# Performance work log

Measured on AMD Instinct MI355X. Metric: run time of the kernel, lower is better.

## Reference

```python
import jax, jax.numpy as jnp
import numpy as np

N_LAYERS = 2
D_MODEL = 1024
D_INNER = 2048  # expand=2
D_STATE = 16
D_CONV = 4
DT_RANK = 64    # ceil(d_model/16)
N_CLASSES = 10
B, L = 4, 1024


def setup_inputs() -> dict:
    key = jax.random.key(0)
    ks = jax.random.split(key, 20)
    s = 0.02
    inp = {
        'x': jax.random.normal(ks[0], (B, L, D_MODEL), jnp.float32),
        'ln1_w': jnp.ones((N_LAYERS, D_MODEL), jnp.float32),
        'ln1_b': jnp.zeros((N_LAYERS, D_MODEL), jnp.float32),
        'in_proj_w': jax.random.normal(ks[1], (N_LAYERS, 2 * D_INNER, D_MODEL), jnp.float32) * s,
        'conv_w': jax.random.normal(ks[2], (N_LAYERS, D_INNER, D_CONV), jnp.float32) * 0.2,
        'conv_b': jnp.zeros((N_LAYERS, D_INNER), jnp.float32),
        'x_proj_w': jax.random.normal(ks[3], (N_LAYERS, DT_RANK + 2 * D_STATE, D_INNER), jnp.float32) * s,
        'dt_proj_w': jax.random.normal(ks[4], (N_LAYERS, D_INNER, DT_RANK), jnp.float32) * 0.1,
        'dt_proj_b': jax.random.normal(ks[5], (N_LAYERS, D_INNER), jnp.float32) * 0.1 - 4.6,  # softplus -> dt ~ 0.01
        'A_log': jnp.broadcast_to(jnp.log(jnp.arange(1, D_STATE + 1, dtype=jnp.float32)), (N_LAYERS, D_INNER, D_STATE)) + 0.0,
        'D_param': jnp.ones((N_LAYERS, D_INNER), jnp.float32),
        'out_proj_w': jax.random.normal(ks[6], (N_LAYERS, D_MODEL, D_INNER), jnp.float32) * s,
        'norm_w': jnp.ones((D_MODEL,), jnp.float32),
        'norm_b': jnp.zeros((D_MODEL,), jnp.float32),
        'head_w': jax.random.normal(ks[7], (N_CLASSES, D_MODEL), jnp.float32) * s,
        'head_b': jnp.zeros((N_CLASSES,), jnp.float32),
    }
    return inp


def _layernorm(x, w, b, eps=1e-5):
    mu = jnp.mean(x, axis=-1, keepdims=True)
    var = jnp.var(x, axis=-1, keepdims=True)
    return (x - mu) * jax.lax.rsqrt(var + eps) * w + b


def _selective_scan(xc, dt, A, Bm, Cm, D):
    # xc, dt: (B, L, D_INNER); Bm, Cm: (B, L, D_STATE); A: (D_INNER, D_STATE); D: (D_INNER,)
    def step(h, inp):
        dt_t, B_t, C_t, xc_t = inp  # (B,C),(B,N),(B,N),(B,C)
        dA = jnp.exp(dt_t[..., None] * A)            # (B, C, N)
        h = dA * h + (dt_t * xc_t)[..., None] * B_t[:, None, :]
        y = jnp.einsum('bcn,bn->bc', h, C_t)
        return h, y

    h0 = jnp.zeros((xc.shape[0], A.shape[0], A.shape[1]), xc.dtype)
    xs = (dt.transpose(1, 0, 2), Bm.transpose(1, 0, 2), Cm.transpose(1, 0, 2), xc.transpose(1, 0, 2))
    _, ys = jax.lax.scan(step, h0, xs)
    y = ys.transpose(1, 0, 2)  # (B, L, C)
    return y + xc * D


def _mamba_layer(x, ln_w, ln_b, in_w, cw, cb, xp_w, dtp_w, dtp_b, A_log, D, out_w):
    h = _layernorm(x, ln_w, ln_b)
    xz = jnp.einsum('bld,ed->ble', h, in_w)          # (B, L, 2*D_INNER)
    x_in, z = jnp.split(xz, 2, axis=-1)
    # causal depthwise conv1d, kernel D_CONV
    xp = jnp.pad(x_in, ((0, 0), (D_CONV - 1, 0), (0, 0)))
    conv = cb
    for k in range(D_CONV):
        conv = conv + cw[:, k] * xp[:, k:k + x_in.shape[1], :]
    xc = jax.nn.silu(conv)
    x_dbl = jnp.einsum('blc,ec->ble', xc, xp_w)
    dt_r = x_dbl[..., :DT_RANK]
    Bm = x_dbl[..., DT_RANK:DT_RANK + D_STATE]
    Cm = x_dbl[..., DT_RANK + D_STATE:]
    dt = jax.nn.softplus(jnp.einsum('blr,cr->blc', dt_r, dtp_w) + dtp_b)
    A = -jnp.exp(A_log)
    y = _selective_scan(xc, dt, A, Bm, Cm, D)
    y = y * jax.nn.silu(z)
    return x + jnp.einsum('blc,dc->bld', y, out_w)


def reference(x, ln1_w, ln1_b, in_proj_w, conv_w, conv_b, x_proj_w, dt_proj_w, dt_proj_b,
              A_log, D_param, out_proj_w, norm_w, norm_b, head_w, head_b):
    for i in range(N_LAYERS):
        x = _mamba_layer(x, ln1_w[i], ln1_b[i], in_proj_w[i], conv_w[i], conv_b[i],
                         x_proj_w[i], dt_proj_w[i], dt_proj_b[i], A_log[i], D_param[i], out_proj_w[i])
    x = _layernorm(x, norm_w, norm_b)
    pooled = jnp.mean(x, axis=1)  # (B, D_MODEL)
    return pooled @ head_w.T + head_b
```

## Files before the change

### kernel.cpp

```cpp
#include <hip/hip_runtime.h>
#include <hip/hip_bf16.h>

#define N_LAYERS 2
#define D_MODEL 1024
#define D_INNER 2048
#define D_STATE 16
#define D_CONV 4
#define DT_RANK 64
#define N_CLASSES 10
#define BB 4
#define LL 1024
#define BL (BB*LL)
#define CH 32
#define CLEN (LL/CH)
#define KS 8
#define KSO 2

typedef __attribute__((ext_vector_type(8))) short bf16x8;
typedef __attribute__((ext_vector_type(8))) unsigned short us8;
typedef __attribute__((ext_vector_type(4))) float f32x4;

typedef const void __attribute__((address_space(1)))* gas_ptr;
typedef void __attribute__((address_space(3)))* las_ptr;
#define GLDS16(g, p) __builtin_amdgcn_global_load_lds((gas_ptr)(g), (las_ptr)(p), 16, 0, 0)

__device__ inline unsigned short rnd_bf16(float x) {
  unsigned u = __float_as_uint(x);
  return (unsigned short)((u + 0x7FFFu + ((u >> 16) & 1u)) >> 16);
}
__device__ inline float b2f(unsigned short u) {
  return __uint_as_float(((unsigned)u) << 16);
}

__global__ __launch_bounds__(256) void round_k(const float* __restrict__ in,
    unsigned short* __restrict__ hi) {
  const int i = blockIdx.x * 256 + threadIdx.x;
  const float4 v = ((const float4*)in)[i];
  ushort4 h4;
  h4.x = rnd_bf16(v.x); h4.y = rnd_bf16(v.y);
  h4.z = rnd_bf16(v.z); h4.w = rnd_bf16(v.w);
  ((ushort4*)hi)[i] = h4;
}

__global__ __launch_bounds__(256) void layernorm_bf16_k(const float* __restrict__ x,
    const float* __restrict__ w, const float* __restrict__ b,
    unsigned short* __restrict__ oh) {
  const int row = blockIdx.x;
  const int t = threadIdx.x;
  const float4 v = *(const float4*)(x + (size_t)row * D_MODEL + t * 4);
  float s = v.x + v.y + v.z + v.w;
  float q = v.x*v.x + v.y*v.y + v.z*v.z + v.w*v.w;
  #pragma unroll
  for (int o = 32; o; o >>= 1) { s += __shfl_down(s, o); q += __shfl_down(q, o); }
  __shared__ float red[8];
  if ((t & 63) == 0) { red[t >> 6] = s; red[4 + (t >> 6)] = q; }
  __syncthreads();
  s = red[0] + red[1] + red[2] + red[3];
  q = red[4] + red[5] + red[6] + red[7];
  const float mean = s * (1.f / D_MODEL);
  const float var  = q * (1.f / D_MODEL) - mean * mean;
  const float rstd = rsqrtf(var + 1e-5f);
  const float4 wv = *(const float4*)(w + t * 4);
  const float4 bv = *(const float4*)(b + t * 4);
  ushort4 h4;
  h4.x = rnd_bf16((v.x - mean) * rstd * wv.x + bv.x);
  h4.y = rnd_bf16((v.y - mean) * rstd * wv.y + bv.y);
  h4.z = rnd_bf16((v.z - mean) * rstd * wv.z + bv.z);
  h4.w = rnd_bf16((v.w - mean) * rstd * wv.w + bv.w);
  ((ushort4*)(oh + (size_t)row * D_MODEL))[t] = h4;
}

template<int OUT>
__global__ __launch_bounds__(256) void oreduce_ln_k(
    const float* __restrict__ part, const float* __restrict__ Xin,
    float* __restrict__ Xout,
    const float* __restrict__ w, const float* __restrict__ b,
    void* __restrict__ out) {
  const int row = blockIdx.x;
  const int t = threadIdx.x;
  float4 v = *(const float4*)(Xin + (size_t)row * D_MODEL + t * 4);
  #pragma unroll
  for (int k = 0; k < KSO; k++) {
    const float4 p = *(const float4*)(part + (size_t)k * BL * D_MODEL
                                      + (size_t)row * D_MODEL + t * 4);
    v.x += p.x; v.y += p.y; v.z += p.z; v.w += p.w;
  }
  *(float4*)(Xout + (size_t)row * D_MODEL + t * 4) = v;
  float s = v.x + v.y + v.z + v.w;
  float q = v.x*v.x + v.y*v.y + v.z*v.z + v.w*v.w;
  #pragma unroll
  for (int o = 32; o; o >>= 1) { s += __shfl_down(s, o); q += __shfl_down(q, o); }
  __shared__ float red[8];
  if ((t & 63) == 0) { red[t >> 6] = s; red[4 + (t >> 6)] = q; }
  __syncthreads();
  s = red[0] + red[1] + red[2] + red[3];
  q = red[4] + red[5] + red[6] + red[7];
  const float mean = s * (1.f / D_MODEL);
  const float var  = q * (1.f / D_MODEL) - mean * mean;
  const float rstd = rsqrtf(var + 1e-5f);
  const float4 wv = *(const float4*)(w + t * 4);
  const float4 bv = *(const float4*)(b + t * 4);
  float4 o4;
  o4.x = (v.x - mean) * rstd * wv.x + bv.x;
  o4.y = (v.y - mean) * rstd * wv.y + bv.y;
  o4.z = (v.z - mean) * rstd * wv.z + bv.z;
  o4.w = (v.w - mean) * rstd * wv.w + bv.w;
  if constexpr (OUT == 0) {
    ushort4 h4;
    h4.x = rnd_bf16(o4.x); h4.y = rnd_bf16(o4.y);
    h4.z = rnd_bf16(o4.z); h4.w = rnd_bf16(o4.w);
    ((ushort4*)((unsigned short*)out + (size_t)row * D_MODEL))[t] = h4;
  } else {
    *(float4*)((float*)out + (size_t)row * D_MODEL + t * 4) = o4;
  }
}

__global__ __launch_bounds__(512) void mfma_gemm256_nt(
    const unsigned short* __restrict__ A, const unsigned short* __restrict__ B,
    unsigned short* __restrict__ C, int K, int ldc) {
  __shared__ unsigned short S[65536];
  const int tid = threadIdx.x;
  const int l = tid & 63;
  const int w = tid >> 6;
  const int wm = w >> 2, wn = w & 3;
  const int bid = blockIdx.y * 16 + blockIdx.x;
  const int x = bid & 7, v = bid >> 3;
  const int bx = (x & 1) * 8 + (v & 7);
  const int by = (x >> 1) * 4 + (v >> 3);
  const int m0 = by * 256, n0 = bx * 256;
  const int nkt = K >> 6;
  const int r8 = (tid >> 3) & 7;
  const int c16s = (tid & 7) ^ r8;

  auto stage1 = [&](int kt, int mat, int half) {
    const unsigned short* base = (mat == 0) ? (A + (size_t)m0 * K)
                                            : (B + (size_t)n0 * K);
    unsigned short* dst = S + ((kt & 1) * 32768 + mat * 16384 + half * 8192);
    #pragma unroll
    for (int e = 0; e < 2; ++e) {
      const int row = half * 128 + e * 64 + (tid >> 3);
      GLDS16(base + (size_t)row * K + kt * 64 + c16s * 8,
             dst + e * 4096 + tid * 8);
    }
  };
  auto stage_full = [&](int kt) {
    stage1(kt, 0, 0); stage1(kt, 0, 1); stage1(kt, 1, 0); stage1(kt, 1, 1);
  };

  stage_full(0);
  if (nkt > 1) stage_full(1);

  f32x4 acc[8][4] = {};
  const int fr = l & 15;
  const int fk8 = l >> 4;

  #pragma unroll 1
  for (int kt = 0; kt < nkt; ++kt) {
    if (kt + 1 < nkt) asm volatile("s_waitcnt vmcnt(8)" ::: "memory");
    else              asm volatile("s_waitcnt vmcnt(0)" ::: "memory");
    __builtin_amdgcn_s_barrier();
    __builtin_amdgcn_sched_barrier(0);
    const unsigned short* SA = S + (kt & 1) * 32768;
    const unsigned short* SB = SA + 16384;
    #pragma unroll
    for (int kk8 = 0; kk8 < 8; kk8 += 4) {
      bf16x8 av[8], bv[4];
      const int c8 = kk8 + fk8;
      #pragma unroll
      for (int i = 0; i < 8; ++i) {
        const int R = wm * 128 + i * 16 + fr;
        av[i] = *(const bf16x8*)&SA[R * 64 + ((c8 ^ (R & 7)) << 3)];
      }
      #pragma unroll
      for (int j = 0; j < 4; ++j) {
        const int R = wn * 64 + j * 16 + fr;
        bv[j] = *(const bf16x8*)&SB[R * 64 + ((c8 ^ (R & 7)) << 3)];
      }
      __builtin_amdgcn_s_setprio(1);
      #pragma unroll
      for (int i = 0; i < 8; ++i)
        #pragma unroll
        for (int j = 0; j < 4; ++j)
          acc[i][j] = __builtin_amdgcn_mfma_f32_16x16x32_bf16(
              av[i], bv[j], acc[i][j], 0, 0, 0);
      __builtin_amdgcn_s_setprio(0);
    }
    __builtin_amdgcn_s_barrier();
    __builtin_amdgcn_sched_barrier(0);
    if (kt + 2 < nkt) stage_full(kt + 2);
  }

  const int orow = (l >> 4) * 4, ocol = l & 15;
  #pragma unroll
  for (int i = 0; i < 8; ++i)
    #pragma unroll
    for (int j = 0; j < 4; ++j)
      #pragma unroll
      for (int r = 0; r < 4; ++r) {
        const int m = m0 + wm * 128 + i * 16 + orow + r;
        const int n = n0 + wn * 64 + j * 16 + ocol;
        C[(size_t)m * ldc + n] = rnd_bf16(acc[i][j][r]);
      }
}

template<int EPI, int KSEG>
__global__ __launch_bounds__(256) void mfma_gemm_nt(
    const unsigned short* __restrict__ Ah, const unsigned short* __restrict__ Bh,
    void* __restrict__ Cv, int M, int N, int K, int ldc,
    const float* __restrict__ bias) {
  __shared__ unsigned short As[128 * 64];
  __shared__ unsigned short Bs[128 * 64];
  const int tid = threadIdx.x;
  const int w = tid >> 6, l = tid & 63;
  const int wr = w >> 1, wc = w & 1;
  const int nbx = gridDim.x;
  const int nwg = nbx * gridDim.y;
  int bid = blockIdx.y * nbx + blockIdx.x;
  bid = (bid & 7) * (nwg >> 3) + (bid >> 3);
  const int st = bid >> 6, wi = bid & 63;
  const int stpr = (nbx >= 8) ? (nbx >> 3) : 1;
  int n0, m0;
  if (nbx >= 8) {
    n0 = ((st % stpr) * 8 + (wi & 7)) * 128;
    m0 = ((st / stpr) * 8 + (wi >> 3)) * 128;
  } else {
    n0 = (bid % nbx) * 128;
    m0 = (bid / nbx) * 128;
  }
  const int kz = (KSEG > 1) ? blockIdx.z : 0;
  const int kbeg = kz * (K / KSEG);
  const int kend = kbeg + K / KSEG;
  const int srow = l >> 3;
  const int scol = (l & 7) * 8;
  const int fr = l & 15;
  const int fk = (l >> 4) * 8;
  f32x4 acc[4][4] = {};

  #pragma unroll 1
  for (int k0 = kbeg; k0 < kend; k0 += 64) {
    __syncthreads();
    #pragma unroll
    for (int it = 0; it < 4; ++it) {
      const int bi = it * 4 + w;
      const int row = bi * 8 + srow;
      GLDS16(Ah + (size_t)(m0 + row) * K + k0 + scol, &As[bi * 512 + l * 8]);
      GLDS16(Bh + (size_t)(n0 + row) * K + k0 + scol, &Bs[bi * 512 + l * 8]);
    }
    __syncthreads();
    #pragma unroll
    for (int kk = 0; kk < 64; kk += 32) {
      bf16x8 a[4], b[4];
      #pragma unroll
      for (int f = 0; f < 4; ++f)
        b[f] = *(const bf16x8*)&Bs[(wc * 64 + f * 16 + fr) * 64 + kk + fk];
      #pragma unroll
      for (int f = 0; f < 4; ++f)
        a[f] = *(const bf16x8*)&As[(wr * 64 + f * 16 + fr) * 64 + kk + fk];
      #pragma unroll
      for (int i = 0; i < 4; ++i)
        #pragma unroll
        for (int j = 0; j < 4; ++j)
          acc[i][j] = __builtin_amdgcn_mfma_f32_16x16x32_bf16(
              a[i], b[j], acc[i][j], 0, 0, 0);
    }
  }
  const int orow = (l >> 4) * 4;
  const int ocol = l & 15;
  if constexpr (EPI == 0 || EPI == 2) {
    unsigned short* Cw = (unsigned short*)Cv;
    #pragma unroll
    for (int i = 0; i < 4; ++i)
      #pragma unroll
      for (int j = 0; j < 4; ++j)
        #pragma unroll
        for (int r = 0; r < 4; ++r) {
          const int m = m0 + wr * 64 + i * 16 + orow + r;
          const int n = n0 + wc * 64 + j * 16 + ocol;
          float vv = acc[i][j][r];
          if constexpr (EPI == 2) {
            vv += bias[n];
            vv = (vv > 20.f) ? vv : log1pf(__expf(vv));
          }
          Cw[(size_t)m * ldc + n] = rnd_bf16(vv);
        }
  } else {
    float* Cw = (float*)Cv + (size_t)kz * M * ldc;
    #pragma unroll
    for (int i = 0; i < 4; ++i)
      #pragma unroll
      for (int j = 0; j < 4; ++j)
        #pragma unroll
        for (int r = 0; r < 4; ++r) {
          const int m = m0 + wr * 64 + i * 16 + orow + r;
          const int n = n0 + wc * 64 + j * 16 + ocol;
          Cw[(size_t)m * ldc + n] = acc[i][j][r];
        }
  }
}

__global__ __launch_bounds__(256) void sgemm_splitk_k(
    const unsigned short* __restrict__ A, const float* __restrict__ B,
    float* __restrict__ part) {
  __shared__ float As[32][64 + 4];
  __shared__ float Bs[32][32 + 4];
  const int tid = threadIdx.x;
  const int n0 = blockIdx.x * 32;
  const int m0 = blockIdx.y * 64;
  const int kz = blockIdx.z;
  const int tn = (tid & 15) * 2;
  const int tm = (tid >> 4) * 4;
  float acc[4][2] = {};
  for (int kb = 0; kb < 256; kb += 32) {
    const int k0 = kz * 256 + kb;
    {
      int r = tid >> 2, c8 = (tid & 3) * 8;
      us8 u = *(const us8*)(A + (size_t)(m0 + r) * D_INNER + k0 + c8);
      #pragma unroll
      for (int j = 0; j < 8; j++) As[c8 + j][r] = b2f((unsigned short)u[j]);
    }
    {
      int r = tid >> 3, c4 = tid & 7;
      float4 v = *(const float4*)(B + (size_t)(n0 + r) * D_INNER + k0 + c4 * 4);
      Bs[c4*4+0][r] = v.x; Bs[c4*4+1][r] = v.y;
      Bs[c4*4+2][r] = v.z; Bs[c4*4+3][r] = v.w;
    }
    __syncthreads();
    #pragma unroll
    for (int k = 0; k < 32; k++) {
      float a[4], bf[2];
      #pragma unroll
      for (int i = 0; i < 4; i++) a[i] = As[k][tm + i];
      bf[0] = Bs[k][tn]; bf[1] = Bs[k][tn + 1];
      #pragma unroll
      for (int i = 0; i < 4; i++) {
        acc[i][0] = fmaf(a[i], bf[0], acc[i][0]);
        acc[i][1] = fmaf(a[i], bf[1], acc[i][1]);
      }
    }
    __syncthreads();
  }
  float* p = part + (size_t)kz * BL * 96;
  #pragma unroll
  for (int i = 0; i < 4; i++) {
    const int m = m0 + tm + i;
    p[(size_t)m * 96 + n0 + tn]     = acc[i][0];
    p[(size_t)m * 96 + n0 + tn + 1] = acc[i][1];
  }
}

__global__ __launch_bounds__(256) void xproj_reduce_k(
    const float* __restrict__ part, unsigned short* __restrict__ dtr,
    float* __restrict__ bc) {
  const int i = blockIdx.x * 256 + threadIdx.x;
  const int m = i / 96, col = i % 96;
  float s = 0.f;
  #pragma unroll
  for (int k = 0; k < KS; k++) s += part[(size_t)k * BL * 96 + i];
  if (col < DT_RANK) dtr[(size_t)m * DT_RANK + col] = rnd_bf16(s);
  else               bc[(size_t)m * 32 + (col - DT_RANK)] = s;
}

__global__ __launch_bounds__(256) void conv_silu_k(
    const unsigned short* __restrict__ xz,
    const float* __restrict__ cw, const float* __restrict__ cb,
    unsigned short* __restrict__ xc) {
  const int gid = blockIdx.x * 256 + threadIdx.x;
  const int c4 = (gid & (D_INNER / 4 - 1)) << 2;
  const int row = gid >> 9;
  const int l = row & (LL - 1);
  const unsigned short* base = xz + (size_t)row * (2 * D_INNER) + c4;
  const float4 w0 = *(const float4*)(cw + (c4 + 0) * 4);
  const float4 w1 = *(const float4*)(cw + (c4 + 1) * 4);
  const float4 w2 = *(const float4*)(cw + (c4 + 2) * 4);
  const float4 w3 = *(const float4*)(cw + (c4 + 3) * 4);
  float4 acc = *(const float4*)(cb + c4);
  ushort4 uv = *(const ushort4*)base;
  acc.x = fmaf(w0.w, b2f(uv.x), acc.x); acc.y = fmaf(w1.w, b2f(uv.y), acc.y);
  acc.z = fmaf(w2.w, b2f(uv.z), acc.z); acc.w = fmaf(w3.w, b2f(uv.w), acc.w);
  if (l >= 1) {
    uv = *(const ushort4*)(base - 2 * D_INNER);
    acc.x = fmaf(w0.z, b2f(uv.x), acc.x); acc.y = fmaf(w1.z, b2f(uv.y), acc.y);
    acc.z = fmaf(w2.z, b2f(uv.z), acc.z); acc.w = fmaf(w3.z, b2f(uv.w), acc.w);
  }
  if (l >= 2) {
    uv = *(const ushort4*)(base - 4 * D_INNER);
    acc.x = fmaf(w0.y, b2f(uv.x), acc.x); acc.y = fmaf(w1.y, b2f(uv.y), acc.y);
    acc.z = fmaf(w2.y, b2f(uv.z), acc.z); acc.w = fmaf(w3.y, b2f(uv.w), acc.w);
  }
  if (l >= 3) {
    uv = *(const ushort4*)(base - 6 * D_INNER);
    acc.x = fmaf(w0.x, b2f(uv.x), acc.x); acc.y = fmaf(w1.x, b2f(uv.y), acc.y);
    acc.z = fmaf(w2.x, b2f(uv.z), acc.z); acc.w = fmaf(w3.x, b2f(uv.w), acc.w);
  }
  ushort4 o4;
  o4.x = rnd_bf16(acc.x / (1.f + __expf(-acc.x)));
  o4.y = rnd_bf16(acc.y / (1.f + __expf(-acc.y)));
  o4.z = rnd_bf16(acc.z / (1.f + __expf(-acc.z)));
  o4.w = rnd_bf16(acc.w / (1.f + __expf(-acc.w)));
  *(ushort4*)(xc + (size_t)row * D_INNER + c4) = o4;
}

__device__ inline void wpowers(float w1, float* P) {
  const float w2 = w1 * w1, w3 = w2 * w1, w4 = w2 * w2;
  const float w5 = w4 * w1, w6 = w4 * w2, w7 = w4 * w3, w8 = w4 * w4;
  P[0] = w1;  P[1] = w2;  P[2] = w3;  P[3] = w4;
  P[4] = w5;  P[5] = w6;  P[6] = w7;  P[7] = w8;
  P[8]  = w8 * w1;  P[9]  = w8 * w2;  P[10] = w8 * w3;  P[11] = w8 * w4;
  P[12] = w8 * w5;  P[13] = w8 * w6;  P[14] = w8 * w7;  P[15] = w8 * w8;
}

__global__ __launch_bounds__(256) void scan_pass1_k(
    const unsigned short* __restrict__ dt, const unsigned short* __restrict__ xc,
    const float* __restrict__ bc, const float* __restrict__ A_log,
    float* __restrict__ hend, float* __restrict__ sumdt) {
  const int c = blockIdx.x * 256 + threadIdx.x;
  const int k = blockIdx.y;
  const int b = blockIdx.z;
  float Ac[D_STATE];
  bool fast = true;
  #pragma unroll
  for (int n = 0; n < D_STATE; n++) {
    Ac[n] = -__expf(A_log[c * D_STATE + n]);
    fast = fast && (fabsf(Ac[n] + (float)(n + 1)) <= 4e-6f * (float)(n + 1));
  }
  float h[D_STATE] = {};
  float sd = 0.f;
  const size_t r0 = (size_t)b * LL + (size_t)k * CLEN;
  const unsigned short* dtp = dt + r0 * D_INNER + c;
  const unsigned short* xcp = xc + r0 * D_INNER + c;
  const float* Bp  = bc + r0 * 32;

  float dtv = b2f(dtp[0]);
  float xv  = b2f(xcp[0]);
  float4 B0 = *(const float4*)(Bp + 0);
  float4 B1 = *(const float4*)(Bp + 4);
  float4 B2 = *(const float4*)(Bp + 8);
  float4 B3 = *(const float4*)(Bp + 12);
  if (fast) {
    for (int l = 0; l < CLEN; l++) {
      const int lp = (l + 1 < CLEN) ? l + 1 : l;
      const float dtv2 = b2f(dtp[(size_t)lp * D_INNER]);
      const float xv2  = b2f(xcp[(size_t)lp * D_INNER]);
      const float4 B0n = *(const float4*)(Bp + (size_t)lp * 32 + 0);
      const float4 B1n = *(const float4*)(Bp + (size_t)lp * 32 + 4);
      const float4 B2n = *(const float4*)(Bp + (size_t)lp * 32 + 8);
      const float4 B3n = *(const float4*)(Bp + (size_t)lp * 32 + 12);
      sd += dtv;
      const float dx = dtv * xv;
      float P[D_STATE];
      wpowers(__expf(-dtv), P);
      const float Bv[D_STATE] = {B0.x,B0.y,B0.z,B0.w, B1.x,B1.y,B1.z,B1.w,
                                 B2.x,B2.y,B2.z,B2.w, B3.x,B3.y,B3.z,B3.w};
      #pragma unroll
      for (int n = 0; n < D_STATE; n++)
        h[n] = fmaf(P[n], h[n], dx * Bv[n]);
      dtv = dtv2; xv = xv2; B0 = B0n; B1 = B1n; B2 = B2n; B3 = B3n;
    }
  } else {
    for (int l = 0; l < CLEN; l++) {
      const int lp = (l + 1 < CLEN) ? l + 1 : l;
      const float dtv2 = b2f(dtp[(size_t)lp * D_INNER]);
      const float xv2  = b2f(xcp[(size_t)lp * D_INNER]);
      const float4 B0n = *(const float4*)(Bp + (size_t)lp * 32 + 0);
      const float4 B1n = *(const float4*)(Bp + (size_t)lp * 32 + 4);
      const float4 B2n = *(const float4*)(Bp + (size_t)lp * 32 + 8);
      const float4 B3n = *(const float4*)(Bp + (size_t)lp * 32 + 12);
      sd += dtv;
      const float dx = dtv * xv;
      const float Bv[D_STATE] = {B0.x,B0.y,B0.z,B0.w, B1.x,B1.y,B1.z,B1.w,
                                 B2.x,B2.y,B2.z,B2.w, B3.x,B3.y,B3.z,B3.w};
      #pragma unroll
      for (int n = 0; n < D_STATE; n++)
        h[n] = fmaf(__expf(dtv * Ac[n]), h[n], dx * Bv[n]);
      dtv = dtv2; xv = xv2; B0 = B0n; B1 = B1n; B2 = B2n; B3 = B3n;
    }
  }
  float* he = hend + (((size_t)(b * CH + k) * D_INNER + c) << 4);
  #pragma unroll
  for (int n = 0; n < D_STATE; n += 4)
    *(float4*)(he + n) = make_float4(h[n], h[n+1], h[n+2], h[n+3]);
  sumdt[(size_t)(b * CH + k) * D_INNER + c] = sd;
}

__global__ __launch_bounds__(256) void scan_fix_k(
    float* __restrict__ hend, const float* __restrict__ sumdt,
    const float* __restrict__ A_log) {
  const int gid = blockIdx.x * 256 + threadIdx.x;
  const int n = gid & 15;
  const int c = (gid >> 4) & (D_INNER - 1);
  const int b = gid >> 15;
  const float Ac = -__expf(A_log[c * D_STATE + n]);
  float hrun = 0.f;
  for (int k = 0; k < CH; k++) {
    const size_t base = (size_t)(b * CH + k) * D_INNER + c;
    const float sd = sumdt[base];
    float* hp = hend + (base << 4) + n;
    const float tmp = *hp;
    *hp = hrun;
    hrun = fmaf(__expf(Ac * sd), hrun, tmp);
  }
}

__global__ __launch_bounds__(256) void scan_pass3_k(
    const unsigned short* __restrict__ dt, const unsigned short* __restrict__ xc,
    const float* __restrict__ bc, const unsigned short* __restrict__ xz,
    const float* __restrict__ h0, const float* __restrict__ A_log,
    const float* __restrict__ Dp, unsigned short* __restrict__ yh) {
  const int c = blockIdx.x * 256 + threadIdx.x;
  const int k = blockIdx.y;
  const int b = blockIdx.z;
  float Ac[D_STATE];
  bool fast = true;
  #pragma unroll
  for (int n = 0; n < D_STATE; n++) {
    Ac[n] = -__expf(A_log[c * D_STATE + n]);
    fast = fast && (fabsf(Ac[n] + (float)(n + 1)) <= 4e-6f * (float)(n + 1));
  }
  const float Dv = Dp[c];
  float h[D_STATE];
  const float* hp = h0 + (((size_t)(b * CH + k) * D_INNER + c) << 4);
  #pragma unroll
  for (int n = 0; n < D_STATE; n += 4) {
    const float4 v = *(const float4*)(hp + n);
    h[n] = v.x; h[n+1] = v.y; h[n+2] = v.z; h[n+3] = v.w;
  }
  const size_t r0 = (size_t)b * LL + (size_t)k * CLEN;
  const unsigned short* dtp = dt + r0 * D_INNER + c;
  const unsigned short* xcp = xc + r0 * D_INNER + c;
  const float* Bp  = bc + r0 * 32;
  const unsigned short* zp = xz + r0 * (size_t)(2 * D_INNER) + D_INNER + c;
  unsigned short* yhp = yh + r0 * D_INNER + c;

  float dtv = b2f(dtp[0]);
  float xv  = b2f(xcp[0]);
  float zv  = b2f(zp[0]);
  float4 B0 = *(const float4*)(Bp + 0);
  float4 B1 = *(const float4*)(Bp + 4);
  float4 B2 = *(const float4*)(Bp + 8);
  float4 B3 = *(const float4*)(Bp + 12);
  float4 C0 = *(const float4*)(Bp + 16);
  float4 C1 = *(const float4*)(Bp + 20);
  float4 C2 = *(const float4*)(Bp + 24);
  float4 C3 = *(const float4*)(Bp + 28);
  if (fast) {
    for (int l = 0; l < CLEN; l++) {
      const int lp = (l + 1 < CLEN) ? l + 1 : l;
      const float dtv2 = b2f(dtp[(size_t)lp * D_INNER]);
      const float xv2  = b2f(xcp[(size_t)lp * D_INNER]);
      const float zv2  = b2f(zp[(size_t)lp * 2 * D_INNER]);
      const float4 B0n = *(const float4*)(Bp + (size_t)lp * 32 + 0);
      const float4 B1n = *(const float4*)(Bp + (size_t)lp * 32 + 4);
      const float4 B2n = *(const float4*)(Bp + (size_t)lp * 32 + 8);
      const float4 B3n = *(const float4*)(Bp + (size_t)lp * 32 + 12);
      const float4 C0n = *(const float4*)(Bp + (size_t)lp * 32 + 16);
      const float4 C1n = *(const float4*)(Bp + (size_t)lp * 32 + 20);
      const float4 C2n = *(const float4*)(Bp + (size_t)lp * 32 + 24);
      const float4 C3n = *(const float4*)(Bp + (size_t)lp * 32 + 28);
      const float dx = dtv * xv;
      float P[D_STATE];
      wpowers(__expf(-dtv), P);
      const float Bv[D_STATE] = {B0.x,B0.y,B0.z,B0.w, B1.x,B1.y,B1.z,B1.w,
                                 B2.x,B2.y,B2.z,B2.w, B3.x,B3.y,B3.z,B3.w};
      const float Cv[D_STATE] = {C0.x,C0.y,C0.z,C0.w, C1.x,C1.y,C1.z,C1.w,
                                 C2.x,C2.y,C2.z,C2.w, C3.x,C3.y,C3.z,C3.w};
      float y = 0.f;
      #pragma unroll
      for (int n = 0; n < D_STATE; n++) {
        h[n] = fmaf(P[n], h[n], dx * Bv[n]);
        y = fmaf(h[n], Cv[n], y);
      }
      y = fmaf(xv, Dv, y);
      y *= zv / (1.f + __expf(-zv));
      yhp[(size_t)l * D_INNER] = rnd_bf16(y);
      dtv = dtv2; xv = xv2; zv = zv2;
      B0 = B0n; B1 = B1n; B2 = B2n; B3 = B3n;
      C0 = C0n; C1 = C1n; C2 = C2n; C3 = C3n;
    }
  } else {
    for (int l = 0; l < CLEN; l++) {
      const int lp = (l + 1 < CLEN) ? l + 1 : l;
      const float dtv2 = b2f(dtp[(size_t)lp * D_INNER]);
      const float xv2  = b2f(xcp[(size_t)lp * D_INNER]);
      const float zv2  = b2f(zp[(size_t)lp * 2 * D_INNER]);
      const float4 B0n = *(const float4*)(Bp + (size_t)lp * 32 + 0);
      const float4 B1n = *(const float4*)(Bp + (size_t)lp * 32 + 4);
      const float4 B2n = *(const float4*)(Bp + (size_t)lp * 32 + 8);
      const float4 B3n = *(const float4*)(Bp + (size_t)lp * 32 + 12);
      const float4 C0n = *(const float4*)(Bp + (size_t)lp * 32 + 16);
      const float4 C1n = *(const float4*)(Bp + (size_t)lp * 32 + 20);
      const float4 C2n = *(const float4*)(Bp + (size_t)lp * 32 + 24);
      const float4 C3n = *(const float4*)(Bp + (size_t)lp * 32 + 28);
      const float dx = dtv * xv;
      const float Bv[D_STATE] = {B0.x,B0.y,B0.z,B0.w, B1.x,B1.y,B1.z,B1.w,
                                 B2.x,B2.y,B2.z,B2.w, B3.x,B3.y,B3.z,B3.w};
      const float Cv[D_STATE] = {C0.x,C0.y,C0.z,C0.w, C1.x,C1.y,C1.z,C1.w,
                                 C2.x,C2.y,C2.z,C2.w, C3.x,C3.y,C3.z,C3.w};
      float y = 0.f;
      #pragma unroll
      for (int n = 0; n < D_STATE; n++) {
        h[n] = fmaf(__expf(dtv * Ac[n]), h[n], dx * Bv[n]);
        y = fmaf(h[n], Cv[n], y);
      }
      y = fmaf(xv, Dv, y);
      y *= zv / (1.f + __expf(-zv));
      yhp[(size_t)l * D_INNER] = rnd_bf16(y);
      dtv = dtv2; xv = xv2; zv = zv2;
      B0 = B0n; B1 = B1n; B2 = B2n; B3 = B3n;
      C0 = C0n; C1 = C1n; C2 = C2n; C3 = C3n;
    }
  }
}

__global__ __launch_bounds__(256) void pool1_k(const float* __restrict__ h,
    float* __restrict__ pp) {
  const int d = blockIdx.x * 256 + threadIdx.x;
  const int b = blockIdx.y;
  const int seg = blockIdx.z;
  float s = 0.f;
  const size_t base = (size_t)b * LL + (size_t)seg * 64;
  for (int l = 0; l < 64; l++) s += h[(base + l) * D_MODEL + d];
  pp[((size_t)(b * 16 + seg)) * D_MODEL + d] = s;
}
__global__ __launch_bounds__(256) void pool2_k(const float* __restrict__ pp,
    float* __restrict__ pooled) {
  const int d = blockIdx.x * 256 + threadIdx.x;
  const int b = blockIdx.y;
  float s = 0.f;
  #pragma unroll
  for (int k = 0; k < 16; k++) s += pp[((size_t)(b * 16 + k)) * D_MODEL + d];
  pooled[b * D_MODEL + d] = s * (1.f / LL);
}

__global__ __launch_bounds__(64) void head_k(const float* __restrict__ pooled,
    const float* __restrict__ hw, const float* __restrict__ hb,
    float* __restrict__ out) {
  const int b = blockIdx.x / N_CLASSES;
  const int j = blockIdx.x % N_CLASSES;
  float s = 0.f;
  for (int k = threadIdx.x; k < D_MODEL; k += 64)
    s = fmaf(pooled[b * D_MODEL + k], hw[j * D_MODEL + k], s);
  #pragma unroll
  for (int o = 32; o; o >>= 1) s += __shfl_down(s, o);
  if (threadIdx.x == 0) out[b * N_CLASSES + j] = s + hb[j];
}

extern "C" void kernel_launch(void* const* d_in, const int* in_sizes, int n_in,
                              void* d_out, int out_size, void* d_ws, size_t ws_size,
                              hipStream_t stream) {
  const float* x0    = (const float*)d_in[0];
  const float* ln1w  = (const float*)d_in[1];
  const float* ln1b  = (const float*)d_in[2];
  const float* inw   = (const float*)d_in[3];
  const float* convw = (const float*)d_in[4];
  const float* convb = (const float*)d_in[5];
  const float* xpw   = (const float*)d_in[6];
  const float* dtpw  = (const float*)d_in[7];
  const float* dtpb  = (const float*)d_in[8];
  const float* Alog  = (const float*)d_in[9];
  const float* Dp    = (const float*)d_in[10];
  const float* outw  = (const float*)d_in[11];
  const float* normw = (const float*)d_in[12];
  const float* normb = (const float*)d_in[13];
  const float* headw = (const float*)d_in[14];
  const float* headb = (const float*)d_in[15];

  float* ws = (float*)d_ws;
  size_t f = 0;
  float* X      = ws + f; f += (size_t)BL * D_MODEL;
  float* xzf    = ws + f; f += (size_t)BL * D_INNER;
  float* bc     = ws + f; f += (size_t)BL * 32;
  float* dty    = ws + f; f += (size_t)BL * D_INNER;
  float* pooled = ws + f; f += 4096;
  float* pooldp = ws + f; f += (size_t)16 * BB * D_MODEL;
  float* xpart  = ws + f; f += (size_t)KS * BL * 96;
  float* hend   = ws + f; f += (size_t)BB * CH * D_INNER * D_STATE;
  float* opart  = ws + f; f += (size_t)KSO * BL * D_MODEL;
  unsigned short* hh  = (unsigned short*)(ws + f); f += (size_t)BL * D_MODEL / 2;
  unsigned short* yh  = (unsigned short*)(ws + f); f += (size_t)BL * D_INNER / 2;
  unsigned short* xcb = (unsigned short*)(ws + f); f += (size_t)BL * D_INNER / 2;
  unsigned short* dtr = (unsigned short*)(ws + f); f += (size_t)BL * DT_RANK / 2;
  unsigned short* wih = (unsigned short*)(ws + f);
  f += (size_t)N_LAYERS * 2 * D_INNER * D_MODEL / 2;
  unsigned short* woh = (unsigned short*)(ws + f);
  f += (size_t)N_LAYERS * D_MODEL * D_INNER / 2;
  unsigned short* wdt = (unsigned short*)(ws + f);
  f += (size_t)N_LAYERS * D_INNER * DT_RANK / 2;
  unsigned short* xz  = (unsigned short*)xzf;
  unsigned short* dtb = (unsigned short*)dty;
  float* sumdt = xpart;

  round_k<<<(N_LAYERS * 2 * D_INNER * D_MODEL) / 1024, 256, 0, stream>>>(inw, wih);
  round_k<<<(N_LAYERS * D_MODEL * D_INNER) / 1024, 256, 0, stream>>>(outw, woh);
  round_k<<<(N_LAYERS * D_INNER * DT_RANK) / 1024, 256, 0, stream>>>(dtpw, wdt);
  layernorm_bf16_k<<<BL, 256, 0, stream>>>(x0, ln1w, ln1b, hh);

  for (int layer = 0; layer < N_LAYERS; ++layer) {
    const unsigned short* wi = wih + (size_t)layer * 2 * D_INNER * D_MODEL;
    const unsigned short* wo = woh + (size_t)layer * D_MODEL * D_INNER;
    const unsigned short* wd = wdt + (size_t)layer * D_INNER * DT_RANK;
    mfma_gemm256_nt<<<dim3(16, 16), 512, 0, stream>>>(
        hh, wi, xz, D_MODEL, 2 * D_INNER);
    conv_silu_k<<<(BL * D_INNER / 4) / 256, 256, 0, stream>>>(
        xz, convw + layer * D_INNER * D_CONV, convb + layer * D_INNER, xcb);
    sgemm_splitk_k<<<dim3(96 / 32, 4096 / 64, KS), 256, 0, stream>>>(
        xcb, xpw + (size_t)layer * 96 * D_INNER, xpart);
    xproj_reduce_k<<<(BL * 96) / 256, 256, 0, stream>>>(xpart, dtr, bc);
    mfma_gemm_nt<2, 1><<<dim3(2048 / 128, 4096 / 128), 256, 0, stream>>>(
        dtr, wd, dtb, BL, D_INNER, DT_RANK, D_INNER, dtpb + layer * D_INNER);
    scan_pass1_k<<<dim3(D_INNER / 256, CH, BB), 256, 0, stream>>>(
        dtb, xcb, bc, Alog + (size_t)layer * D_INNER * D_STATE, hend, sumdt);
    scan_fix_k<<<(BB * D_INNER * D_STATE) / 256, 256, 0, stream>>>(
        hend, sumdt, Alog + (size_t)layer * D_INNER * D_STATE);
    scan_pass3_k<<<dim3(D_INNER / 256, CH, BB), 256, 0, stream>>>(
        dtb, xcb, bc, xz, hend, Alog + (size_t)layer * D_INNER * D_STATE,
        Dp + layer * D_INNER, yh);
    mfma_gemm_nt<1, KSO><<<dim3(1024 / 128, 4096 / 128, KSO), 256, 0, stream>>>(
        yh, wo, opart, BL, D_MODEL, D_INNER, D_MODEL, nullptr);
    const float* Xin = (layer == 0) ? x0 : X;
    if (layer + 1 < N_LAYERS) {
      oreduce_ln_k<0><<<BL, 256, 0, stream>>>(
          opart, Xin, X, ln1w + (layer + 1) * D_MODEL,
          ln1b + (layer + 1) * D_MODEL, hh);
    } else {
      oreduce_ln_k<1><<<BL, 256, 0, stream>>>(opart, Xin, X, normw, normb, dty);
    }
  }

  pool1_k<<<dim3(D_MODEL / 256, BB, 16), 256, 0, stream>>>(dty, pooldp);
  pool2_k<<<dim3(D_MODEL / 256, BB), 256, 0, stream>>>(pooldp, pooled);
  head_k<<<BB * N_CLASSES, 64, 0, stream>>>(pooled, headw, headb, (float*)d_out);
}
```

Baseline: 504.9 us.

## Move out_proj onto 256-tile split-K GEMM and overlap next-stage loads with MFMAs

The 256x256 MFMA GEMM is templated to support a float split-K epilogue and an unremapped grid, and out_proj now uses it with four K-segments instead of the 128-tile kernel with two. Inside the main loop, the second k-half's LDS fragments are loaded first, then the barrier and next-stage global-to-LDS loads are issued before the second MFMA batch, so loads overlap compute. The workspace is reordered so the larger split-K partial buffer aliases the xz/xcb/hend region, which is dead by then. The cost is double the fp32 partial write and reduce traffic.

```diff
diff --git a/kernel.cpp b/kernel.cpp
--- a/kernel.cpp
+++ b/kernel.cpp
@@ -14,7 +14,7 @@
 #define CH 32
 #define CLEN (LL/CH)
 #define KS 8
-#define KSO 2
+#define KSO 4
 
 typedef __attribute__((ext_vector_type(8))) short bf16x8;
 typedef __attribute__((ext_vector_type(8))) unsigned short us8;
@@ -115,20 +115,28 @@
   }
 }
 
+template<int EPI, int KSEG, int REMAP>
 __global__ __launch_bounds__(512) void mfma_gemm256_nt(
     const unsigned short* __restrict__ A, const unsigned short* __restrict__ B,
-    unsigned short* __restrict__ C, int K, int ldc) {
+    void* __restrict__ Cv, int M, int N, int K, int ldc) {
   __shared__ unsigned short S[65536];
   const int tid = threadIdx.x;
   const int l = tid & 63;
   const int w = tid >> 6;
   const int wm = w >> 2, wn = w & 3;
-  const int bid = blockIdx.y * 16 + blockIdx.x;
-  const int x = bid & 7, v = bid >> 3;
-  const int bx = (x & 1) * 8 + (v & 7);
-  const int by = (x >> 1) * 4 + (v >> 3);
+  int bx, by;
+  if constexpr (REMAP == 1) {
+    const int bid = blockIdx.y * 16 + blockIdx.x;
+    const int x = bid & 7, v = bid >> 3;
+    bx = (x & 1) * 8 + (v & 7);
+    by = (x >> 1) * 4 + (v >> 3);
+  } else {
+    bx = blockIdx.x; by = blockIdx.y;
+  }
   const int m0 = by * 256, n0 = bx * 256;
-  const int nkt = K >> 6;
+  const int kseg = K / KSEG;
+  const int kbeg = (KSEG > 1) ? blockIdx.z * kseg : 0;
+  const int nkt = kseg >> 6;
   const int r8 = (tid >> 3) & 7;
   const int c16s = (tid & 7) ^ r8;
 
@@ -139,7 +147,7 @@
     #pragma unroll
     for (int e = 0; e < 2; ++e) {
       const int row = half * 128 + e * 64 + (tid >> 3);
-      GLDS16(base + (size_t)row * K + kt * 64 + c16s * 8,
+      GLDS16(base + (size_t)row * K + kbeg + kt * 64 + c16s * 8,
              dst + e * 4096 + tid * 8);
     }
   };
@@ -162,10 +170,9 @@
     __builtin_amdgcn_sched_barrier(0);
     const unsigned short* SA = S + (kt & 1) * 32768;
     const unsigned short* SB = SA + 16384;
-    #pragma unroll
-    for (int kk8 = 0; kk8 < 8; kk8 += 4) {
-      bf16x8 av[8], bv[4];
-      const int c8 = kk8 + fk8;
+    bf16x8 av[8], bv[4];
+    {
+      const int c8 = fk8;
       #pragma unroll
       for (int i = 0; i < 8; ++i) {
         const int R = wm * 128 + i * 16 + fr;
@@ -185,22 +192,59 @@
               av[i], bv[j], acc[i][j], 0, 0, 0);
       __builtin_amdgcn_s_setprio(0);
     }
-    __builtin_amdgcn_s_barrier();
-    __builtin_amdgcn_sched_barrier(0);
-    if (kt + 2 < nkt) stage_full(kt + 2);
+    {
+      const int c8 = 4 + fk8;
+      #pragma unroll
+      for (int i = 0; i < 8; ++i) {
+        const int R = wm * 128 + i * 16 + fr;
+        av[i] = *(const bf16x8*)&SA[R * 64 + ((c8 ^ (R & 7)) << 3)];
+      }
+      #pragma unroll
+      for (int j = 0; j < 4; ++j) {
+        const int R = wn * 64 + j * 16 + fr;
+        bv[j] = *(const bf16x8*)&SB[R * 64 + ((c8 ^ (R & 7)) << 3)];
+      }
+      asm volatile("s_waitcnt lgkmcnt(0)" ::: "memory");
+      __builtin_amdgcn_s_barrier();
+      __builtin_amdgcn_sched_barrier(0);
+      if (kt + 2 < nkt) stage_full(kt + 2);
+      __builtin_amdgcn_s_setprio(1);
+      #pragma unroll
+      for (int i = 0; i < 8; ++i)
+        #pragma unroll
+        for (int j = 0; j < 4; ++j)
+          acc[i][j] = __builtin_amdgcn_mfma_f32_16x16x32_bf16(
+              av[i], bv[j], acc[i][j], 0, 0, 0);
+      __builtin_amdgcn_s_setprio(0);
+    }
   }
 
   const int orow = (l >> 4) * 4, ocol = l & 15;
-  #pragma unroll
-  for (int i = 0; i < 8; ++i)
+  if constexpr (EPI == 0) {
+    unsigned short* C = (unsigned short*)Cv;
     #pragma unroll
-    for (int j = 0; j < 4; ++j)
-      #pragma unroll
-      for (int r = 0; r < 4; ++r) {
-        const int m = m0 + wm * 128 + i * 16 + orow + r;
-        const int n = n0 + wn * 64 + j * 16 + ocol;
-        C[(size_t)m * ldc + n] = rnd_bf16(acc[i][j][r]);
-      }
+    for (int i = 0; i < 8; ++i)
+      #pragma unroll
+      for (int j = 0; j < 4; ++j)
+        #pragma unroll
+        for (int r = 0; r < 4; ++r) {
+          const int m = m0 + wm * 128 + i * 16 + orow + r;
+          const int n = n0 + wn * 64 + j * 16 + ocol;
+          C[(size_t)m * ldc + n] = rnd_bf16(acc[i][j][r]);
+        }
+  } else {
+    float* C = (float*)Cv + (size_t)blockIdx.z * M * ldc;
+    #pragma unroll
+    for (int i = 0; i < 8; ++i)
+      #pragma unroll
+      for (int j = 0; j < 4; ++j)
+        #pragma unroll
+        for (int r = 0; r < 4; ++r) {
+          const int m = m0 + wm * 128 + i * 16 + orow + r;
+          const int n = n0 + wn * 64 + j * 16 + ocol;
+          C[(size_t)m * ldc + n] = acc[i][j][r];
+        }
+  }
 }
 
 template<int EPI, int KSEG>
@@ -668,16 +712,17 @@
   size_t f = 0;
   float* X      = ws + f; f += (size_t)BL * D_MODEL;
   float* xzf    = ws + f; f += (size_t)BL * D_INNER;
+  unsigned short* xcb = (unsigned short*)(ws + f);
+  f += (size_t)BL * D_INNER / 2;
+  float* hend   = ws + f; f += (size_t)BB * CH * D_INNER * D_STATE;
+  float* opart  = xzf;
   float* bc     = ws + f; f += (size_t)BL * 32;
   float* dty    = ws + f; f += (size_t)BL * D_INNER;
   float* pooled = ws + f; f += 4096;
   float* pooldp = ws + f; f += (size_t)16 * BB * D_MODEL;
   float* xpart  = ws + f; f += (size_t)KS * BL * 96;
-  float* hend   = ws + f; f += (size_t)BB * CH * D_INNER * D_STATE;
-  float* opart  = ws + f; f += (size_t)KSO * BL * D_MODEL;
   unsigned short* hh  = (unsigned short*)(ws + f); f += (size_t)BL * D_MODEL / 2;
   unsigned short* yh  = (unsigned short*)(ws + f); f += (size_t)BL * D_INNER / 2;
-  unsigned short* xcb = (unsigned short*)(ws + f); f += (size_t)BL * D_INNER / 2;
   unsigned short* dtr = (unsigned short*)(ws + f); f += (size_t)BL * DT_RANK / 2;
   unsigned short* wih = (unsigned short*)(ws + f);
   f += (size_t)N_LAYERS * 2 * D_INNER * D_MODEL / 2;
@@ -698,8 +743,8 @@
     const unsigned short* wi = wih + (size_t)layer * 2 * D_INNER * D_MODEL;
     const unsigned short* wo = woh + (size_t)layer * D_MODEL * D_INNER;
     const unsigned short* wd = wdt + (size_t)layer * D_INNER * DT_RANK;
-    mfma_gemm256_nt<<<dim3(16, 16), 512, 0, stream>>>(
-        hh, wi, xz, D_MODEL, 2 * D_INNER);
+    mfma_gemm256_nt<0, 1, 1><<<dim3(16, 16), 512, 0, stream>>>(
+        hh, wi, xz, BL, 2 * D_INNER, D_MODEL, 2 * D_INNER);
     conv_silu_k<<<(BL * D_INNER / 4) / 256, 256, 0, stream>>>(
         xz, convw + layer * D_INNER * D_CONV, convb + layer * D_INNER, xcb);
     sgemm_splitk_k<<<dim3(96 / 32, 4096 / 64, KS), 256, 0, stream>>>(
@@ -714,8 +759,9 @@
     scan_pass3_k<<<dim3(D_INNER / 256, CH, BB), 256, 0, stream>>>(
         dtb, xcb, bc, xz, hend, Alog + (size_t)layer * D_INNER * D_STATE,
         Dp + layer * D_INNER, yh);
-    mfma_gemm_nt<1, KSO><<<dim3(1024 / 128, 4096 / 128, KSO), 256, 0, stream>>>(
-        yh, wo, opart, BL, D_MODEL, D_INNER, D_MODEL, nullptr);
+    mfma_gemm256_nt<1, KSO, 0><<<dim3(1024 / 256, 4096 / 256, KSO), 512, 0,
+                                 stream>>>(
+        yh, wo, opart, BL, D_MODEL, D_INNER, D_MODEL);
     const float* Xin = (layer == 0) ? x0 : X;
     if (layer + 1 < N_LAYERS) {
       oreduce_ln_k<0><<<BL, 256, 0, stream>>>(
```

New measurement: 512.5 us (median of 5 runs). About the same (+1.5%).
